# Kernel tuning notes

Measured on AMD Instinct MI355X. Metric: run time of the kernel, lower is better.

The kernel has to match this reference:

```python
import jax, jax.numpy as jnp
import numpy as np

ALPHA = 0.2          # LeakyReLU negative slope
NEG_BIG = -9e15      # mask value from the original code


def setup_inputs() -> dict:
    key = jax.random.key(0)
    k1, k2, k3, k4, k5 = jax.random.split(key, 5)
    N, Fin, Fout, C = 8192, 2048, 256, 8
    x = jax.random.normal(k1, (N, Fin), dtype=jnp.float32)
    # xavier_uniform-ish scale for params
    W = jax.random.normal(k2, (C, Fin, Fout), dtype=jnp.float32) / np.sqrt(Fin).astype(np.float32)
    a = jax.random.normal(k3, (2 * Fout, 1), dtype=jnp.float32) / np.sqrt(2 * Fout).astype(np.float32)
    cam_ids = jax.random.randint(k4, (N,), 0, C, dtype=jnp.int32)
    adj = jax.random.randint(k5, (N, N), 0, 2, dtype=jnp.int32)
    return {"x": x, "W": W, "a": a, "cam_ids": cam_ids, "adj": adj}


def reference(x, W, a, cam_ids, adj):
    N = x.shape[0]
    Fout = W.shape[-1]
    # per-node camera-specific projection: h[i] = x[i] @ W[cam_ids[i]]
    # compute all-camera projections (N, C, Fout) then gather per node;
    # avoids materializing W[cam_ids] of shape (N, Fin, Fout)
    hs = jnp.einsum('nd,cdo->nco', x, W)                       # (N, C, Fout)
    h = jnp.take_along_axis(hs, cam_ids[:, None, None], axis=1)[:, 0, :]  # (N, Fout)
    # e_ij = leakyrelu([h_i, h_j] @ a) = leakyrelu(h_i.a1 + h_j.a2)
    a1 = a[:Fout, 0]
    a2 = a[Fout:, 0]
    e = jax.nn.leaky_relu((h @ a1)[:, None] + (h @ a2)[None, :], ALPHA)  # (N, N)
    att = jnp.where(adj > 0, e, jnp.float32(NEG_BIG))
    att = jax.nn.softmax(att, axis=1)
    # dropout is identity at eval (p applied only in training)
    h_prime = att @ h                                          # (N, Fout)
    return jax.nn.elu(h_prime)                                 # concat=True -> ELU
```

## Files before the change

### kernel.cpp

```cpp
#include <hip/hip_runtime.h>

#define NR 8192
#define FIN 2048
#define FOUT 256
#define ALPHA 0.2f
#define NTMAX 136
#define KS 4
#define KLEN 512
#define NSTEPS 16
#define JC 4
#define NJ 2048

typedef float f32x4 __attribute__((ext_vector_type(4)));
typedef float f32x16 __attribute__((ext_vector_type(16)));
typedef int i32x4 __attribute__((ext_vector_type(4)));
typedef unsigned int u32x4 __attribute__((ext_vector_type(4)));
typedef unsigned short u16x4 __attribute__((ext_vector_type(4)));
typedef unsigned short u16x8 __attribute__((ext_vector_type(8)));
typedef __bf16 bf16x8 __attribute__((ext_vector_type(8)));
typedef _Float16 f16x8 __attribute__((ext_vector_type(8)));

__device__ __forceinline__ unsigned short f2bf(float f){
  unsigned u = __float_as_uint(f);
  return (unsigned short)((u + 0x7fffu + ((u >> 16) & 1u)) >> 16);
}
__device__ __forceinline__ float bf2f(unsigned short b){
  return __uint_as_float(((unsigned)b) << 16);
}
__device__ __forceinline__ void gload16(const void* gptr, void* lptr){
  __builtin_amdgcn_global_load_lds(
      (const __attribute__((address_space(1))) unsigned int*)gptr,
      (__attribute__((address_space(3))) unsigned int*)lptr, 16, 0, 0);
}

__global__ __launch_bounds__(256) void k_wth(const float* __restrict__ W,
                                             _Float16* __restrict__ WhT){
  __shared__ _Float16 tl[64][72];
  int t = threadIdx.x;
  int item = blockIdx.x;
  int k0 = (item & 31) << 6;
  int n0 = ((item >> 5) & 3) << 6;
  int c = item >> 7;
  {
    int kk = t >> 2, nq = (t & 3)*16;
    const float* src = W + ((size_t)c*FIN + k0 + kk)*FOUT + n0 + nq;
    #pragma unroll
    for (int q = 0; q < 4; q++){
      f32x4 v = *(const f32x4*)(src + q*4);
      #pragma unroll
      for (int e = 0; e < 4; e++) tl[nq + q*4 + e][kk] = (_Float16)v[e];
    }
  }
  __syncthreads();
  {
    int nn = t >> 2, kq = (t & 3)*16;
    union { u32x4 v[2]; _Float16 s[16]; } buf;
    #pragma unroll
    for (int e = 0; e < 16; e++) buf.s[e] = tl[nn][kq + e];
    u32x4* dst = (u32x4*)(WhT + ((size_t)c*FOUT + n0 + nn)*FIN + k0 + kq);
    dst[0] = buf.v[0]; dst[1] = buf.v[1];
  }
}

__global__ void k_bucket(const int* __restrict__ cam, int* __restrict__ prows,
                         int* __restrict__ tileCam){
  __shared__ int cnt[256][8];
  __shared__ int scnt[8];
  __shared__ int tst[9];
  int t = threadIdx.x;
  int loc[8];
  #pragma unroll
  for (int c = 0; c < 8; c++) loc[c] = 0;
  for (int k = 0; k < 32; k++) loc[cam[t*32 + k] & 7]++;
  #pragma unroll
  for (int c = 0; c < 8; c++) cnt[t][c] = loc[c];
  __syncthreads();
  if (t < 8){
    int s = 0;
    for (int i = 0; i < 256; i++){ int v = cnt[i][t]; cnt[i][t] = s; s += v; }
    scnt[t] = s;
  }
  __syncthreads();
  if (t == 0){
    int ts = 0;
    for (int c = 0; c < 8; c++){ tst[c] = ts; ts += (scnt[c] + 63) >> 6; }
    tst[8] = ts;
  }
  __syncthreads();
  for (int s = t; s < NTMAX*64; s += 256) prows[s] = -1;
  if (t < NTMAX){
    int tc = -1, te = tst[8];
    if (t < te){
      #pragma unroll
      for (int c = 0; c < 8; c++)
        if (t >= tst[c] && t < tst[c+1]) tc = c;
    }
    tileCam[t] = tc;
  }
  __syncthreads();
  int off[8];
  #pragma unroll
  for (int c = 0; c < 8; c++) off[c] = cnt[t][c];
  for (int k = 0; k < 32; k++){
    int n = t*32 + k; int c = cam[n] & 7;
    int slot = off[c]++;
    prows[(tst[c] + (slot >> 6))*64 + (slot & 63)] = n;
  }
}

__global__ __launch_bounds__(256, 3) void k_gmm(const float* __restrict__ x,
    const _Float16* __restrict__ WhT, const int* __restrict__ tileCam,
    const int* __restrict__ prows, float* __restrict__ partial){
  __shared__ __align__(16) char smem[41728];
  int item = blockIdx.x;
  int tile = item >> 2, ks = item & 3;
  int camc = tileCam[tile];
  if (camc < 0) return;
  _Float16* ab = (_Float16*)smem;
  int* rows  = (int*)(smem + 40960);
  int* growL = (int*)(smem + 41216);
  int t = threadIdx.x;
  if (t < 64){
    int r = prows[tile*64 + t];
    rows[t] = r; growL[t] = (r < 0) ? 0 : r;
  }
  __syncthreads();
  int lane = t & 63, w = t >> 6;
  int k0 = ks * KLEN;
  int wr = w >> 1, wc = w & 1;
  int rA = ((t >> 6) & 1)*32 + (t & 31);
  int koffA = (t >> 7)*16 + ((t >> 5) & 1)*8;
  const float* srcA = x + (size_t)growL[rA]*FIN + k0 + koffA;
  const _Float16* srcB[4];
  #pragma unroll
  for (int q = 0; q < 4; q++){
    int c2 = q*256 + t;
    int colg = ((c2 >> 6) & 7)*32 + (t & 31);
    srcB[q] = WhT + ((size_t)camc*FOUT + colg)*FIN + k0
            + (c2 >> 9)*16 + ((t >> 5) & 1)*8;
  }
  f32x16 acc[4];
  #pragma unroll
  for (int nb = 0; nb < 4; nb++)
    #pragma unroll
    for (int r = 0; r < 16; r++) acc[nb][r] = 0.f;
  int cur = 0;
  {
    f32x4 a0 = *(const f32x4*)srcA;
    f32x4 a1 = *(const f32x4*)(srcA + 4);
    #pragma unroll
    for (int q = 0; q < 4; q++) gload16(srcB[q], &ab[2048 + (q*256 + t)*8]);
    f16x8 hv;
    #pragma unroll
    for (int e = 0; e < 4; e++){ hv[e] = (_Float16)a0[e]; hv[4+e] = (_Float16)a1[e]; }
    *(f16x8*)&ab[t*8] = hv;
  }
  __syncthreads();
  for (int s = 0; s < NSTEPS; s++){
    bool have = (s + 1 < NSTEPS);
    int adv = have ? (s + 1)*32 : 0;
    f32x4 na0 = *(const f32x4*)(srcA + adv);
    f32x4 na1 = *(const f32x4*)(srcA + adv + 4);
    if (have){
      #pragma unroll
      for (int q = 0; q < 4; q++)
        gload16(srcB[q] + adv, &ab[(cur ^ 1)*10240 + 2048 + (q*256 + t)*8]);
    }
    const _Float16* base = ab + cur*10240;
    f16x8 af[2]; f16x8 bfr[2][4];
    #pragma unroll
    for (int kk = 0; kk < 2; kk++){
      af[kk] = *(const f16x8*)(base + ((kk*2 + wr)*64 + lane)*8);
      #pragma unroll
      for (int nb = 0; nb < 4; nb++)
        bfr[kk][nb] = *(const f16x8*)(base + 2048 + ((kk*8 + wc*4 + nb)*64 + lane)*8);
    }
    #pragma unroll
    for (int kk = 0; kk < 2; kk++)
      #pragma unroll
      for (int nb = 0; nb < 4; nb++)
        acc[nb] = __builtin_amdgcn_mfma_f32_32x32x16_f16(af[kk], bfr[kk][nb], acc[nb], 0, 0, 0);
    if (have){
      f16x8 hv;
      #pragma unroll
      for (int e = 0; e < 4; e++){ hv[e] = (_Float16)na0[e]; hv[4+e] = (_Float16)na1[e]; }
      *(f16x8*)&ab[(cur ^ 1)*10240 + t*8] = hv;
    }
    __syncthreads();
    cur ^= 1;
  }
  int colb = wc*128;
  #pragma unroll
  for (int nb = 0; nb < 4; nb++){
    #pragma unroll
    for (int r = 0; r < 16; r++){
      int rowl = wr*32 + (r & 3) + 8*(r >> 2) + 4*(lane >> 5);
      int grow = rows[rowl];
      if (grow >= 0)
        partial[((size_t)ks*NR + grow)*FOUT + colb + nb*32 + (lane & 31)] = acc[nb][r];
    }
  }
}

__global__ __launch_bounds__(256) void k_hsumT(const float* __restrict__ partial,
    const float* __restrict__ a, float* __restrict__ s1, float* __restrict__ s2,
    float* __restrict__ bm, unsigned short* __restrict__ hT){
  __shared__ __align__(16) char smem[36096];
  unsigned short* sums = (unsigned short*)smem;
  float* a1l = (float*)(smem + 33792);
  float* a2l = (float*)(smem + 34816);
  float* redv = (float*)(smem + 35840);
  int blk = blockIdx.x, t = threadIdx.x;
  int w = t >> 6, lane = t & 63;
  int r0 = blk*64;
  a1l[t] = a[t]; a2l[t] = a[FOUT + t];
  __syncthreads();
  float bmax = -3.0e38f;
  #pragma unroll
  for (int rep = 0; rep < 16; rep++){
    int row = rep*4 + w;
    const float* pp = partial + (size_t)(r0 + row)*FOUT + lane*4;
    f32x4 s; s[0] = s[1] = s[2] = s[3] = 0.f;
    #pragma unroll
    for (int ks = 0; ks < KS; ks++)
      s += *(const f32x4*)(pp + (size_t)ks*NR*FOUT);
    u16x4 pk;
    #pragma unroll
    for (int e = 0; e < 4; e++) pk[e] = f2bf(s[e]);
    *(u16x4*)&sums[row*264 + lane*4] = pk;
    f32x4 a1v = *(const f32x4*)&a1l[lane*4];
    f32x4 a2v = *(const f32x4*)&a2l[lane*4];
    float p1 = 0.f, p2 = 0.f;
    #pragma unroll
    for (int e = 0; e < 4; e++){ p1 = fmaf(s[e], a1v[e], p1); p2 = fmaf(s[e], a2v[e], p2); }
    #pragma unroll
    for (int off2 = 32; off2 > 0; off2 >>= 1){
      p1 += __shfl_xor(p1, off2);
      p2 += __shfl_xor(p2, off2);
    }
    if (lane == 0){
      s1[r0 + row] = p1; s2[r0 + row] = p2;
      bmax = fmaxf(bmax, p2);
    }
  }
  if (lane == 0) redv[w] = bmax;
  __syncthreads();
  if (t == 0)
    bm[blk] = fmaxf(fmaxf(redv[0], redv[1]), fmaxf(redv[2], redv[3]));
  int c = t;
  #pragma unroll
  for (int q = 0; q < 8; q++){
    u16x8 v;
    #pragma unroll
    for (int e = 0; e < 8; e++) v[e] = sums[(q*8 + e)*264 + c];
    *(u16x8*)(hT + (size_t)c*NR + r0 + q*8) = v;
  }
}

__global__ __launch_bounds__(512, 4) void k_flash(const int* __restrict__ adj,
    const float* __restrict__ s1g, const float* __restrict__ s2g,
    const float* __restrict__ bm, const unsigned short* __restrict__ hT,
    float* __restrict__ hp, float* __restrict__ Dp){
  __shared__ __align__(16) unsigned short hTl[256*64];
  __shared__ __align__(16) unsigned short pl[64][72];
  __shared__ float s1l[64], ml[64], Dl[64], red[8];
  int blk = blockIdx.x, t = threadIdx.x;
  int w = t >> 6, lane = t & 63;
  int it = blk & 127, jc = blk >> 7;
  int i0 = it*64;
  int jbase = jc * NJ;
  {
    float v = (t < 128) ? bm[t] : -3.0e38f;
    #pragma unroll
    for (int off = 32; off > 0; off >>= 1) v = fmaxf(v, __shfl_xor(v, off));
    if (lane == 0) red[w] = v;
  }
  __syncthreads();
  if (t == 0){
    float v = red[0];
    #pragma unroll
    for (int k = 1; k < 8; k++) v = fmaxf(v, red[k]);
    red[0] = v;
  }
  __syncthreads();
  float maxS2 = red[0];
  if (t < 64){
    float sv = s1g[i0 + t];
    s1l[t] = sv;
    float mm = sv + maxS2;
    ml[t] = fmaxf(mm, ALPHA*mm);
  }
  __syncthreads();
  int il = t >> 3, tj = t & 7;
  float s1i = s1l[il], mi = ml[il];
  float Dacc = 0.f;
  f32x16 acc0, acc1;
  #pragma unroll
  for (int k = 0; k < 16; k++){ acc0[k] = 0.f; acc1[k] = 0.f; }
  const unsigned short* hsrc[4];
  int ldst[4];
  #pragma unroll
  for (int q = 0; q < 4; q++){
    int g = t + 512*q;
    int row = g >> 3, part = g & 7;
    hsrc[q] = hT + (size_t)row*NR + jbase + part*8;
    ldst[q] = row*64 + ((part ^ (row & 7))*8);
  }
  const int* arow = adj + (size_t)(i0 + il)*NR + jbase + tj*8;
  u32x4 hch[4];
  #pragma unroll
  for (int q = 0; q < 4; q++) hch[q] = *(const u32x4*)hsrc[q];
  i32x4 ad0 = __builtin_nontemporal_load((const i32x4*)arow);
  i32x4 ad1 = __builtin_nontemporal_load(((const i32x4*)arow) + 1);
  f32x4 s20 = *(const f32x4*)(s2g + jbase + tj*8);
  f32x4 s21 = *(const f32x4*)(s2g + jbase + tj*8 + 4);
  for (int jt = 0; jt < NJ; jt += 64){
    u16x8 pu;
    float Dloc = 0.f;
    #pragma unroll
    for (int e = 0; e < 4; e++){
      float e0 = s1i + s20[e]; e0 = fmaxf(e0, ALPHA*e0);
      float p0 = (ad0[e] > 0) ? __expf(e0 - mi) : 0.f;
      unsigned short b0 = f2bf(p0); pu[e] = b0; Dloc += bf2f(b0);
      float e1 = s1i + s21[e]; e1 = fmaxf(e1, ALPHA*e1);
      float p1 = (ad1[e] > 0) ? __expf(e1 - mi) : 0.f;
      unsigned short b1 = f2bf(p1); pu[e + 4] = b1; Dloc += bf2f(b1);
    }
    Dacc += Dloc;
    *(u16x8*)&pl[il][tj*8] = pu;
    #pragma unroll
    for (int q = 0; q < 4; q++) *(u32x4*)&hTl[ldst[q]] = hch[q];
    __syncthreads();
    if (jt + 64 < NJ){
      #pragma unroll
      for (int q = 0; q < 4; q++){
        hsrc[q] += 64;
        hch[q] = *(const u32x4*)hsrc[q];
      }
      arow += 64;
      ad0 = __builtin_nontemporal_load((const i32x4*)arow);
      ad1 = __builtin_nontemporal_load(((const i32x4*)arow) + 1);
      s20 = *(const f32x4*)(s2g + jbase + jt + 64 + tj*8);
      s21 = *(const f32x4*)(s2g + jbase + jt + 64 + tj*8 + 4);
    }
    int nrow = w*32 + (lane & 31);
    #pragma unroll
    for (int ks = 0; ks < 4; ks++){
      int p = ks*2 + (lane >> 5);
      bf16x8 B = *(const bf16x8*)&hTl[nrow*64 + ((p ^ (nrow & 7))*8)];
      int koff = ks*16 + (lane >> 5)*8;
      bf16x8 a0 = *(const bf16x8*)&pl[lane & 31][koff];
      acc0 = __builtin_amdgcn_mfma_f32_32x32x16_bf16(a0, B, acc0, 0, 0, 0);
      bf16x8 a1 = *(const bf16x8*)&pl[32 + (lane & 31)][koff];
      acc1 = __builtin_amdgcn_mfma_f32_32x32x16_bf16(a1, B, acc1, 0, 0, 0);
    }
    __syncthreads();
  }
  Dacc += __shfl_xor(Dacc, 1);
  Dacc += __shfl_xor(Dacc, 2);
  Dacc += __shfl_xor(Dacc, 4);
  if (tj == 0) Dl[il] = Dacc;
  __syncthreads();
  if (t < 64) Dp[(size_t)jc*NR + i0 + t] = Dl[t];
  float* hpb = hp + (size_t)jc*NR*FOUT;
  int col = w*32 + (lane & 31);
  #pragma unroll
  for (int r = 0; r < 16; r++){
    int rowl = (r & 3) + 8*(r >> 2) + 4*(lane >> 5);
    hpb[(size_t)(i0 + rowl)*FOUT + col] = acc0[r];
    hpb[(size_t)(i0 + 32 + rowl)*FOUT + col] = acc1[r];
  }
}

__global__ __launch_bounds__(256) void k_final(const float* __restrict__ hp,
    const float* __restrict__ Dp, float* __restrict__ out){
  int g = blockIdx.x*256 + threadIdx.x;
  int i = g >> 6, cg4 = (g & 63)*4;
  f32x4 s; s[0] = s[1] = s[2] = s[3] = 0.f;
  float D = 0.f;
  #pragma unroll
  for (int jc = 0; jc < JC; jc++){
    s += *(const f32x4*)(hp + ((size_t)jc*NR + i)*FOUT + cg4);
    D += Dp[(size_t)jc*NR + i];
  }
  float inv = (D > 0.f) ? 1.f / D : 0.f;
  f32x4 o;
  #pragma unroll
  for (int e = 0; e < 4; e++){
    float v = s[e]*inv;
    o[e] = (v > 0.f) ? v : expm1f(v);
  }
  *(f32x4*)(out + (size_t)i*FOUT + cg4) = o;
}

extern "C" void kernel_launch(void* const* d_in, const int* in_sizes, int n_in,
                              void* d_out, int out_size, void* d_ws, size_t ws_size,
                              hipStream_t stream){
  (void)in_sizes; (void)n_in; (void)out_size; (void)ws_size;
  const float* x   = (const float*)d_in[0];
  const float* W   = (const float*)d_in[1];
  const float* a   = (const float*)d_in[2];
  const int*   cam = (const int*)d_in[3];
  const int*   adj = (const int*)d_in[4];
  float* out = (float*)d_out;
  char* ws = (char*)d_ws;

  size_t off = 0;
  auto alloc = [&](size_t b) -> void* {
    void* p = ws + off; off = (off + b + 255) & ~(size_t)255; return p;
  };
  int* tileCam  = (int*)alloc((size_t)NTMAX*4);
  int* prows    = (int*)alloc((size_t)NTMAX*64*4);
  _Float16* WhT = (_Float16*)alloc((size_t)8*FIN*FOUT*2);
  unsigned short* hT = (unsigned short*)alloc((size_t)NR*FOUT*2);
  float* s1 = (float*)alloc((size_t)NR*4);
  float* s2 = (float*)alloc((size_t)NR*4);
  float* bm = (float*)alloc(128*4);
  float* Dp = (float*)alloc((size_t)JC*NR*4);
  float* partial = (float*)alloc((size_t)KS*NR*FOUT*4);
  float* hp = partial;

  hipLaunchKernelGGL(k_wth, dim3(1024), dim3(256), 0, stream, W, WhT);
  hipLaunchKernelGGL(k_bucket, dim3(1), dim3(256), 0, stream,
                     cam, prows, tileCam);
  hipLaunchKernelGGL(k_gmm, dim3(NTMAX*4), dim3(256), 0, stream,
                     x, WhT, tileCam, prows, partial);
  hipLaunchKernelGGL(k_hsumT, dim3(128), dim3(256), 0, stream,
                     partial, a, s1, s2, bm, hT);
  hipLaunchKernelGGL(k_flash, dim3(512), dim3(512), 0, stream,
                     adj, s1, s2, bm, hT, hp, Dp);
  hipLaunchKernelGGL(k_final, dim3((NR*FOUT/4)/256), dim3(256), 0, stream,
                     hp, Dp, out);
}
```

Before: 199.4 us.

## Merge preprocessing kernels and fuse attention stages into a cooperative grid-synced kernel

Weight transpose and camera bucketing now run as one launch, with one extra block doing the bucketing. The hsum/transpose, flash-attention and final normalisation stages become phases of a single cooperative kernel separated by grid.sync(). The hsum phase moves to 512-thread blocks and the final phase processes two elements per thread. The aim is to cut kernel launch gaps and tail idling between the dependent stages. The cost is grid-wide barriers and the need for all 512 blocks to be resident at once; if the cooperative launch fails, it falls back to separate launches.

```diff
diff --git a/kernel.cpp b/kernel.cpp
--- a/kernel.cpp
+++ b/kernel.cpp
@@ -1,4 +1,7 @@
 #include <hip/hip_runtime.h>
+#include <hip/hip_cooperative_groups.h>
+
+namespace cg = cooperative_groups;
 
 #define NR 8192
 #define FIN 2048
@@ -33,11 +36,9 @@
       (__attribute__((address_space(3))) unsigned int*)lptr, 16, 0, 0);
 }
 
-__global__ __launch_bounds__(256) void k_wth(const float* __restrict__ W,
-                                             _Float16* __restrict__ WhT){
-  __shared__ _Float16 tl[64][72];
-  int t = threadIdx.x;
-  int item = blockIdx.x;
+__device__ __forceinline__ void phase_wth(int item, int t,
+    const float* __restrict__ W, _Float16* __restrict__ WhT, char* smem){
+  _Float16* tl = (_Float16*)smem;
   int k0 = (item & 31) << 6;
   int n0 = ((item >> 5) & 3) << 6;
   int c = item >> 7;
@@ -48,7 +49,7 @@
     for (int q = 0; q < 4; q++){
       f32x4 v = *(const f32x4*)(src + q*4);
       #pragma unroll
-      for (int e = 0; e < 4; e++) tl[nq + q*4 + e][kk] = (_Float16)v[e];
+      for (int e = 0; e < 4; e++) tl[(nq + q*4 + e)*72 + kk] = (_Float16)v[e];
     }
   }
   __syncthreads();
@@ -56,18 +57,17 @@
     int nn = t >> 2, kq = (t & 3)*16;
     union { u32x4 v[2]; _Float16 s[16]; } buf;
     #pragma unroll
-    for (int e = 0; e < 16; e++) buf.s[e] = tl[nn][kq + e];
+    for (int e = 0; e < 16; e++) buf.s[e] = tl[nn*72 + kq + e];
     u32x4* dst = (u32x4*)(WhT + ((size_t)c*FOUT + n0 + nn)*FIN + k0 + kq);
     dst[0] = buf.v[0]; dst[1] = buf.v[1];
   }
 }
 
-__global__ void k_bucket(const int* __restrict__ cam, int* __restrict__ prows,
-                         int* __restrict__ tileCam){
-  __shared__ int cnt[256][8];
-  __shared__ int scnt[8];
-  __shared__ int tst[9];
-  int t = threadIdx.x;
+__device__ __forceinline__ void phase_bucket(int t, const int* __restrict__ cam,
+    int* __restrict__ prows, int* __restrict__ tileCam, char* smem){
+  int (*cnt)[8] = (int(*)[8])smem;
+  int* scnt = (int*)(smem + 8192);
+  int* tst  = (int*)(smem + 8224);
   int loc[8];
   #pragma unroll
   for (int c = 0; c < 8; c++) loc[c] = 0;
@@ -106,6 +106,15 @@
     int slot = off[c]++;
     prows[(tst[c] + (slot >> 6))*64 + (slot & 63)] = n;
   }
+}
+
+__global__ __launch_bounds__(256) void k_pre(const float* __restrict__ W,
+    _Float16* __restrict__ WhT, const int* __restrict__ cam,
+    int* __restrict__ prows, int* __restrict__ tileCam){
+  __shared__ __align__(16) char smem[9216];
+  int blk = blockIdx.x, t = threadIdx.x;
+  if (blk < 1024) phase_wth(blk, t, W, WhT, smem);
+  else            phase_bucket(t, cam, prows, tileCam, smem);
 }
 
 __global__ __launch_bounds__(256, 3) void k_gmm(const float* __restrict__ x,
@@ -202,23 +211,22 @@
   }
 }
 
-__global__ __launch_bounds__(256) void k_hsumT(const float* __restrict__ partial,
-    const float* __restrict__ a, float* __restrict__ s1, float* __restrict__ s2,
-    float* __restrict__ bm, unsigned short* __restrict__ hT){
-  __shared__ __align__(16) char smem[36096];
+__device__ __forceinline__ void phase_hsumT512(int blk, int t,
+    const float* __restrict__ partial, const float* __restrict__ a,
+    float* __restrict__ s1, float* __restrict__ s2, float* __restrict__ bm,
+    unsigned short* __restrict__ hT, char* smem){
   unsigned short* sums = (unsigned short*)smem;
   float* a1l = (float*)(smem + 33792);
   float* a2l = (float*)(smem + 34816);
   float* redv = (float*)(smem + 35840);
-  int blk = blockIdx.x, t = threadIdx.x;
   int w = t >> 6, lane = t & 63;
   int r0 = blk*64;
-  a1l[t] = a[t]; a2l[t] = a[FOUT + t];
+  if (t < 256){ a1l[t] = a[t]; a2l[t] = a[FOUT + t]; }
   __syncthreads();
   float bmax = -3.0e38f;
   #pragma unroll
-  for (int rep = 0; rep < 16; rep++){
-    int row = rep*4 + w;
+  for (int rep = 0; rep < 8; rep++){
+    int row = rep*8 + w;
     const float* pp = partial + (size_t)(r0 + row)*FOUT + lane*4;
     f32x4 s; s[0] = s[1] = s[2] = s[3] = 0.f;
     #pragma unroll
@@ -245,26 +253,33 @@
   }
   if (lane == 0) redv[w] = bmax;
   __syncthreads();
-  if (t == 0)
-    bm[blk] = fmaxf(fmaxf(redv[0], redv[1]), fmaxf(redv[2], redv[3]));
-  int c = t;
-  #pragma unroll
-  for (int q = 0; q < 8; q++){
+  if (t == 0){
+    float v = redv[0];
+    #pragma unroll
+    for (int k = 1; k < 8; k++) v = fmaxf(v, redv[k]);
+    bm[blk] = v;
+  }
+  int c = t & 255, qb = (t >> 8)*4;
+  #pragma unroll
+  for (int q = 0; q < 4; q++){
     u16x8 v;
     #pragma unroll
-    for (int e = 0; e < 8; e++) v[e] = sums[(q*8 + e)*264 + c];
-    *(u16x8*)(hT + (size_t)c*NR + r0 + q*8) = v;
-  }
-}
-
-__global__ __launch_bounds__(512, 4) void k_flash(const int* __restrict__ adj,
-    const float* __restrict__ s1g, const float* __restrict__ s2g,
-    const float* __restrict__ bm, const unsigned short* __restrict__ hT,
-    float* __restrict__ hp, float* __restrict__ Dp){
-  __shared__ __align__(16) unsigned short hTl[256*64];
-  __shared__ __align__(16) unsigned short pl[64][72];
-  __shared__ float s1l[64], ml[64], Dl[64], red[8];
-  int blk = blockIdx.x, t = threadIdx.x;
+    for (int e = 0; e < 8; e++) v[e] = sums[((qb + q)*8 + e)*264 + c];
+    *(u16x8*)(hT + (size_t)c*NR + r0 + (qb + q)*8) = v;
+  }
+}
+
+__device__ __forceinline__ void phase_flash(int blk, int t,
+    const int* __restrict__ adj, const float* __restrict__ s1g,
+    const float* __restrict__ s2g, const float* __restrict__ bm,
+    const unsigned short* __restrict__ hT, float* __restrict__ hp,
+    float* __restrict__ Dp, char* smem){
+  unsigned short* hTl = (unsigned short*)smem;
+  unsigned short (*pl)[72] = (unsigned short(*)[72])(smem + 32768);
+  float* s1l = (float*)(smem + 41984);
+  float* ml  = (float*)(smem + 42240);
+  float* Dl  = (float*)(smem + 42496);
+  float* red = (float*)(smem + 42752);
   int w = t >> 6, lane = t & 63;
   int it = blk & 127, jc = blk >> 7;
   int i0 = it*64;
@@ -372,25 +387,59 @@
   }
 }
 
-__global__ __launch_bounds__(256) void k_final(const float* __restrict__ hp,
-    const float* __restrict__ Dp, float* __restrict__ out){
-  int g = blockIdx.x*256 + threadIdx.x;
-  int i = g >> 6, cg4 = (g & 63)*4;
-  f32x4 s; s[0] = s[1] = s[2] = s[3] = 0.f;
-  float D = 0.f;
-  #pragma unroll
-  for (int jc = 0; jc < JC; jc++){
-    s += *(const f32x4*)(hp + ((size_t)jc*NR + i)*FOUT + cg4);
-    D += Dp[(size_t)jc*NR + i];
-  }
-  float inv = (D > 0.f) ? 1.f / D : 0.f;
-  f32x4 o;
-  #pragma unroll
-  for (int e = 0; e < 4; e++){
-    float v = s[e]*inv;
-    o[e] = (v > 0.f) ? v : expm1f(v);
-  }
-  *(f32x4*)(out + (size_t)i*FOUT + cg4) = o;
+__device__ __forceinline__ void phase_final2(int gid,
+    const float* __restrict__ hp, const float* __restrict__ Dp,
+    float* __restrict__ out){
+  #pragma unroll
+  for (int rep = 0; rep < 2; rep++){
+    int u = rep*262144 + gid;
+    int i = u >> 6, cg4 = (u & 63)*4;
+    f32x4 s; s[0] = s[1] = s[2] = s[3] = 0.f;
+    float D = 0.f;
+    #pragma unroll
+    for (int jc = 0; jc < JC; jc++){
+      s += *(const f32x4*)(hp + ((size_t)jc*NR + i)*FOUT + cg4);
+      D += Dp[(size_t)jc*NR + i];
+    }
+    float inv = (D > 0.f) ? 1.f / D : 0.f;
+    f32x4 o;
+    #pragma unroll
+    for (int e = 0; e < 4; e++){
+      float v = s[e]*inv;
+      o[e] = (v > 0.f) ? v : expm1f(v);
+    }
+    *(f32x4*)(out + (size_t)i*FOUT + cg4) = o;
+  }
+}
+
+__global__ __launch_bounds__(512, 4) void kCoop(const float* partial,
+    const float* a, float* s1, float* s2, float* bm, unsigned short* hT,
+    const int* adj, float* hp, float* Dp, float* out){
+  __shared__ __align__(16) char smem[43008];
+  cg::grid_group grid = cg::this_grid();
+  int blk = blockIdx.x, t = threadIdx.x;
+  if (blk < 128) phase_hsumT512(blk, t, partial, a, s1, s2, bm, hT, smem);
+  __syncthreads();
+  grid.sync();
+  phase_flash(blk, t, adj, s1, s2, bm, hT, hp, Dp, smem);
+  grid.sync();
+  phase_final2(blk*512 + t, hp, Dp, out);
+}
+
+__global__ __launch_bounds__(512) void kF_hsumT(const float* partial,
+    const float* a, float* s1, float* s2, float* bm, unsigned short* hT){
+  __shared__ __align__(16) char smem[36096];
+  phase_hsumT512(blockIdx.x, threadIdx.x, partial, a, s1, s2, bm, hT, smem);
+}
+__global__ __launch_bounds__(512, 4) void kF_flash(const int* adj,
+    const float* s1, const float* s2, const float* bm,
+    const unsigned short* hT, float* hp, float* Dp){
+  __shared__ __align__(16) char smem[43008];
+  phase_flash(blockIdx.x, threadIdx.x, adj, s1, s2, bm, hT, hp, Dp, smem);
+}
+__global__ __launch_bounds__(512) void kF_final(const float* hp,
+    const float* Dp, float* out){
+  phase_final2(blockIdx.x*512 + threadIdx.x, hp, Dp, out);
 }
 
 extern "C" void kernel_launch(void* const* d_in, const int* in_sizes, int n_in,
@@ -420,15 +469,23 @@
   float* partial = (float*)alloc((size_t)KS*NR*FOUT*4);
   float* hp = partial;
 
-  hipLaunchKernelGGL(k_wth, dim3(1024), dim3(256), 0, stream, W, WhT);
-  hipLaunchKernelGGL(k_bucket, dim3(1), dim3(256), 0, stream,
-                     cam, prows, tileCam);
+  hipLaunchKernelGGL(k_pre, dim3(1025), dim3(256), 0, stream,
+                     W, WhT, cam, prows, tileCam);
   hipLaunchKernelGGL(k_gmm, dim3(NTMAX*4), dim3(256), 0, stream,
                      x, WhT, tileCam, prows, partial);
-  hipLaunchKernelGGL(k_hsumT, dim3(128), dim3(256), 0, stream,
-                     partial, a, s1, s2, bm, hT);
-  hipLaunchKernelGGL(k_flash, dim3(512), dim3(512), 0, stream,
-                     adj, s1, s2, bm, hT, hp, Dp);
-  hipLaunchKernelGGL(k_final, dim3((NR*FOUT/4)/256), dim3(256), 0, stream,
-                     hp, Dp, out);
-}
+  {
+    void* args[] = { (void*)&partial, (void*)&a, (void*)&s1, (void*)&s2,
+                     (void*)&bm, (void*)&hT, (void*)&adj, (void*)&hp,
+                     (void*)&Dp, (void*)&out };
+    hipError_t rc = hipLaunchCooperativeKernel((const void*)kCoop, dim3(512),
+                                               dim3(512), args, 0, stream);
+    if (rc != hipSuccess){
+      hipLaunchKernelGGL(kF_hsumT, dim3(128), dim3(512), 0, stream,
+                         partial, a, s1, s2, bm, hT);
+      hipLaunchKernelGGL(kF_flash, dim3(512), dim3(512), 0, stream,
+                         adj, s1, s2, bm, hT, hp, Dp);
+      hipLaunchKernelGGL(kF_final, dim3(512), dim3(512), 0, stream,
+                         hp, Dp, out);
+    }
+  }
+}
```

Measured after the change: 319.6 us. +60.3%, slower.

## Split flash attention over eight key chunks with swizzled P tile and fewer barriers

Applied to the files above, without the earlier changes.

Doubles the number of key-column chunks in the attention kernel (1024 blocks of 512 threads, each covering 1024 columns) and raises the occupancy hint. It also swizzles the P tile in LDS instead of padding it, computes the global max and per-row values directly from global memory without the startup barriers, and writes the row sums without an LDS round trip. The aim is to fill more CUs and cut sync and bank-conflict overhead. In exchange the partial-output buffer doubles in size, the final reduction reads twice as much, and register pressure is tighter at the higher occupancy target.

```diff
diff --git a/kernel.cpp b/kernel.cpp
--- a/kernel.cpp
+++ b/kernel.cpp
@@ -8,8 +8,8 @@
 #define KS 4
 #define KLEN 512
 #define NSTEPS 16
-#define JC 4
-#define NJ 2048
+#define JC 8
+#define NJ 1024
 
 typedef float f32x4 __attribute__((ext_vector_type(4)));
 typedef float f32x16 __attribute__((ext_vector_type(16)));
@@ -257,42 +257,27 @@
   }
 }
 
-__global__ __launch_bounds__(512, 4) void k_flash(const int* __restrict__ adj,
+__global__ __launch_bounds__(512, 8) void k_flash(const int* __restrict__ adj,
     const float* __restrict__ s1g, const float* __restrict__ s2g,
     const float* __restrict__ bm, const unsigned short* __restrict__ hT,
     float* __restrict__ hp, float* __restrict__ Dp){
   __shared__ __align__(16) unsigned short hTl[256*64];
-  __shared__ __align__(16) unsigned short pl[64][72];
-  __shared__ float s1l[64], ml[64], Dl[64], red[8];
+  __shared__ __align__(16) unsigned short pl[64*64];
   int blk = blockIdx.x, t = threadIdx.x;
   int w = t >> 6, lane = t & 63;
   int it = blk & 127, jc = blk >> 7;
   int i0 = it*64;
   int jbase = jc * NJ;
-  {
-    float v = (t < 128) ? bm[t] : -3.0e38f;
-    #pragma unroll
-    for (int off = 32; off > 0; off >>= 1) v = fmaxf(v, __shfl_xor(v, off));
-    if (lane == 0) red[w] = v;
-  }
-  __syncthreads();
-  if (t == 0){
-    float v = red[0];
-    #pragma unroll
-    for (int k = 1; k < 8; k++) v = fmaxf(v, red[k]);
-    red[0] = v;
-  }
-  __syncthreads();
-  float maxS2 = red[0];
-  if (t < 64){
-    float sv = s1g[i0 + t];
-    s1l[t] = sv;
-    float mm = sv + maxS2;
-    ml[t] = fmaxf(mm, ALPHA*mm);
-  }
-  __syncthreads();
+  float maxS2 = -3.0e38f;
+  #pragma unroll
+  for (int q = 0; q < 32; q++){
+    f32x4 v = *(const f32x4*)(bm + q*4);
+    maxS2 = fmaxf(fmaxf(maxS2, fmaxf(v[0], v[1])), fmaxf(v[2], v[3]));
+  }
   int il = t >> 3, tj = t & 7;
-  float s1i = s1l[il], mi = ml[il];
+  float s1i = s1g[i0 + il];
+  float mm = s1i + maxS2;
+  float mi = fmaxf(mm, ALPHA*mm);
   float Dacc = 0.f;
   f32x16 acc0, acc1;
   #pragma unroll
@@ -306,6 +291,7 @@
     hsrc[q] = hT + (size_t)row*NR + jbase + part*8;
     ldst[q] = row*64 + ((part ^ (row & 7))*8);
   }
+  int plw = il*64 + ((tj ^ (il & 7))*8);
   const int* arow = adj + (size_t)(i0 + il)*NR + jbase + tj*8;
   u32x4 hch[4];
   #pragma unroll
@@ -327,16 +313,13 @@
       unsigned short b1 = f2bf(p1); pu[e + 4] = b1; Dloc += bf2f(b1);
     }
     Dacc += Dloc;
-    *(u16x8*)&pl[il][tj*8] = pu;
+    *(u16x8*)&pl[plw] = pu;
     #pragma unroll
     for (int q = 0; q < 4; q++) *(u32x4*)&hTl[ldst[q]] = hch[q];
     __syncthreads();
     if (jt + 64 < NJ){
       #pragma unroll
-      for (int q = 0; q < 4; q++){
-        hsrc[q] += 64;
-        hch[q] = *(const u32x4*)hsrc[q];
-      }
+      for (int q = 0; q < 4; q++) hch[q] = *(const u32x4*)(hsrc[q] + jt + 64);
       arow += 64;
       ad0 = __builtin_nontemporal_load((const i32x4*)arow);
       ad1 = __builtin_nontemporal_load(((const i32x4*)arow) + 1);
@@ -344,14 +327,14 @@
       s21 = *(const f32x4*)(s2g + jbase + jt + 64 + tj*8 + 4);
     }
     int nrow = w*32 + (lane & 31);
+    int r = lane & 31;
     #pragma unroll
     for (int ks = 0; ks < 4; ks++){
       int p = ks*2 + (lane >> 5);
       bf16x8 B = *(const bf16x8*)&hTl[nrow*64 + ((p ^ (nrow & 7))*8)];
-      int koff = ks*16 + (lane >> 5)*8;
-      bf16x8 a0 = *(const bf16x8*)&pl[lane & 31][koff];
+      bf16x8 a0 = *(const bf16x8*)&pl[r*64 + ((p ^ (r & 7))*8)];
       acc0 = __builtin_amdgcn_mfma_f32_32x32x16_bf16(a0, B, acc0, 0, 0, 0);
-      bf16x8 a1 = *(const bf16x8*)&pl[32 + (lane & 31)][koff];
+      bf16x8 a1 = *(const bf16x8*)&pl[(32 + r)*64 + ((p ^ (r & 7))*8)];
       acc1 = __builtin_amdgcn_mfma_f32_32x32x16_bf16(a1, B, acc1, 0, 0, 0);
     }
     __syncthreads();
@@ -359,16 +342,14 @@
   Dacc += __shfl_xor(Dacc, 1);
   Dacc += __shfl_xor(Dacc, 2);
   Dacc += __shfl_xor(Dacc, 4);
-  if (tj == 0) Dl[il] = Dacc;
-  __syncthreads();
-  if (t < 64) Dp[(size_t)jc*NR + i0 + t] = Dl[t];
+  if (tj == 0) Dp[(size_t)jc*NR + i0 + il] = Dacc;
   float* hpb = hp + (size_t)jc*NR*FOUT;
   int col = w*32 + (lane & 31);
   #pragma unroll
-  for (int r = 0; r < 16; r++){
-    int rowl = (r & 3) + 8*(r >> 2) + 4*(lane >> 5);
-    hpb[(size_t)(i0 + rowl)*FOUT + col] = acc0[r];
-    hpb[(size_t)(i0 + 32 + rowl)*FOUT + col] = acc1[r];
+  for (int r2 = 0; r2 < 16; r2++){
+    int rowl = (r2 & 3) + 8*(r2 >> 2) + 4*(lane >> 5);
+    hpb[(size_t)(i0 + rowl)*FOUT + col] = acc0[r2];
+    hpb[(size_t)(i0 + 32 + rowl)*FOUT + col] = acc1[r2];
   }
 }
 
@@ -417,8 +398,11 @@
   float* s2 = (float*)alloc((size_t)NR*4);
   float* bm = (float*)alloc(128*4);
   float* Dp = (float*)alloc((size_t)JC*NR*4);
-  float* partial = (float*)alloc((size_t)KS*NR*FOUT*4);
-  float* hp = partial;
+  size_t sh1 = (size_t)KS*NR*FOUT*4;
+  size_t sh2 = (size_t)JC*NR*FOUT*4;
+  void* shared = alloc(sh1 > sh2 ? sh1 : sh2);
+  float* partial = (float*)shared;
+  float* hp      = (float*)shared;
 
   hipLaunchKernelGGL(k_wth, dim3(1024), dim3(256), 0, stream, W, WhT);
   hipLaunchKernelGGL(k_bucket, dim3(1), dim3(256), 0, stream,
@@ -427,7 +411,7 @@
                      x, WhT, tileCam, prows, partial);
   hipLaunchKernelGGL(k_hsumT, dim3(128), dim3(256), 0, stream,
                      partial, a, s1, s2, bm, hT);
-  hipLaunchKernelGGL(k_flash, dim3(512), dim3(512), 0, stream,
+  hipLaunchKernelGGL(k_flash, dim3(1024), dim3(512), 0, stream,
                      adj, s1, s2, bm, hT, hp, Dp);
   hipLaunchKernelGGL(k_final, dim3((NR*FOUT/4)/256), dim3(256), 0, stream,
                      hp, Dp, out);
```

Result: slower. 685.0 us (+243.5%).

## Halve flash attention row tile to 32 rows with 256-thread blocks

Applied to the files above, without the earlier changes.

The flash kernel now processes 32 query rows per block with 4 waves instead of 64 rows with 8 waves, doubling the grid to 1024 blocks. Each wave now computes two 32-column output slabs sharing one A fragment, and each thread loads 8 hT chunks per step instead of 4. This raises the block count for better CU occupancy and load balance, but each block re-streams the full hT tile for only half the rows, doubling hT traffic per output row.

```diff
diff --git a/kernel.cpp b/kernel.cpp
--- a/kernel.cpp
+++ b/kernel.cpp
@@ -257,17 +257,17 @@
   }
 }
 
-__global__ __launch_bounds__(512, 4) void k_flash(const int* __restrict__ adj,
+__global__ __launch_bounds__(256, 4) void k_flash(const int* __restrict__ adj,
     const float* __restrict__ s1g, const float* __restrict__ s2g,
     const float* __restrict__ bm, const unsigned short* __restrict__ hT,
     float* __restrict__ hp, float* __restrict__ Dp){
   __shared__ __align__(16) unsigned short hTl[256*64];
-  __shared__ __align__(16) unsigned short pl[64][72];
-  __shared__ float s1l[64], ml[64], Dl[64], red[8];
+  __shared__ __align__(16) unsigned short pl[32][72];
+  __shared__ float s1l[32], ml[32], red[4];
   int blk = blockIdx.x, t = threadIdx.x;
   int w = t >> 6, lane = t & 63;
-  int it = blk & 127, jc = blk >> 7;
-  int i0 = it*64;
+  int it = blk & 255, jc = blk >> 8;
+  int i0 = it*32;
   int jbase = jc * NJ;
   {
     float v = (t < 128) ? bm[t] : -3.0e38f;
@@ -276,15 +276,11 @@
     if (lane == 0) red[w] = v;
   }
   __syncthreads();
-  if (t == 0){
-    float v = red[0];
-    #pragma unroll
-    for (int k = 1; k < 8; k++) v = fmaxf(v, red[k]);
-    red[0] = v;
-  }
+  if (t == 0)
+    red[0] = fmaxf(fmaxf(red[0], red[1]), fmaxf(red[2], red[3]));
   __syncthreads();
   float maxS2 = red[0];
-  if (t < 64){
+  if (t < 32){
     float sv = s1g[i0 + t];
     s1l[t] = sv;
     float mm = sv + maxS2;
@@ -297,19 +293,14 @@
   f32x16 acc0, acc1;
   #pragma unroll
   for (int k = 0; k < 16; k++){ acc0[k] = 0.f; acc1[k] = 0.f; }
-  const unsigned short* hsrc[4];
-  int ldst[4];
-  #pragma unroll
-  for (int q = 0; q < 4; q++){
-    int g = t + 512*q;
-    int row = g >> 3, part = g & 7;
-    hsrc[q] = hT + (size_t)row*NR + jbase + part*8;
-    ldst[q] = row*64 + ((part ^ (row & 7))*8);
-  }
+  int r0s = t >> 3, part = t & 7;
+  const unsigned short* hbase = hT + (size_t)r0s*NR + jbase + part*8;
+  int ldst0 = r0s*64 + ((part ^ (r0s & 7))*8);
   const int* arow = adj + (size_t)(i0 + il)*NR + jbase + tj*8;
-  u32x4 hch[4];
-  #pragma unroll
-  for (int q = 0; q < 4; q++) hch[q] = *(const u32x4*)hsrc[q];
+  u32x4 hch[8];
+  #pragma unroll
+  for (int q = 0; q < 8; q++)
+    hch[q] = *(const u32x4*)(hbase + (size_t)q*(32*NR));
   i32x4 ad0 = __builtin_nontemporal_load((const i32x4*)arow);
   i32x4 ad1 = __builtin_nontemporal_load(((const i32x4*)arow) + 1);
   f32x4 s20 = *(const f32x4*)(s2g + jbase + tj*8);
@@ -329,46 +320,48 @@
     Dacc += Dloc;
     *(u16x8*)&pl[il][tj*8] = pu;
     #pragma unroll
-    for (int q = 0; q < 4; q++) *(u32x4*)&hTl[ldst[q]] = hch[q];
+    for (int q = 0; q < 8; q++) *(u32x4*)&hTl[ldst0 + q*2048] = hch[q];
     __syncthreads();
     if (jt + 64 < NJ){
-      #pragma unroll
-      for (int q = 0; q < 4; q++){
-        hsrc[q] += 64;
-        hch[q] = *(const u32x4*)hsrc[q];
-      }
+      int jn = jt + 64;
+      #pragma unroll
+      for (int q = 0; q < 8; q++)
+        hch[q] = *(const u32x4*)(hbase + jn + (size_t)q*(32*NR));
       arow += 64;
       ad0 = __builtin_nontemporal_load((const i32x4*)arow);
       ad1 = __builtin_nontemporal_load(((const i32x4*)arow) + 1);
-      s20 = *(const f32x4*)(s2g + jbase + jt + 64 + tj*8);
-      s21 = *(const f32x4*)(s2g + jbase + jt + 64 + tj*8 + 4);
-    }
-    int nrow = w*32 + (lane & 31);
+      s20 = *(const f32x4*)(s2g + jbase + jn + tj*8);
+      s21 = *(const f32x4*)(s2g + jbase + jn + tj*8 + 4);
+    }
+    int r = lane & 31, hi = lane >> 5;
+    int nrow0 = w*64 + r;
+    int nrow1 = w*64 + 32 + r;
     #pragma unroll
     for (int ks = 0; ks < 4; ks++){
-      int p = ks*2 + (lane >> 5);
-      bf16x8 B = *(const bf16x8*)&hTl[nrow*64 + ((p ^ (nrow & 7))*8)];
-      int koff = ks*16 + (lane >> 5)*8;
-      bf16x8 a0 = *(const bf16x8*)&pl[lane & 31][koff];
-      acc0 = __builtin_amdgcn_mfma_f32_32x32x16_bf16(a0, B, acc0, 0, 0, 0);
-      bf16x8 a1 = *(const bf16x8*)&pl[32 + (lane & 31)][koff];
-      acc1 = __builtin_amdgcn_mfma_f32_32x32x16_bf16(a1, B, acc1, 0, 0, 0);
+      int p = ks*2 + hi;
+      int koff = ks*16 + hi*8;
+      bf16x8 a = *(const bf16x8*)&pl[r][koff];
+      bf16x8 B0 = *(const bf16x8*)&hTl[nrow0*64 + ((p ^ (nrow0 & 7))*8)];
+      acc0 = __builtin_amdgcn_mfma_f32_32x32x16_bf16(a, B0, acc0, 0, 0, 0);
+      bf16x8 B1 = *(const bf16x8*)&hTl[nrow1*64 + ((p ^ (nrow1 & 7))*8)];
+      acc1 = __builtin_amdgcn_mfma_f32_32x32x16_bf16(a, B1, acc1, 0, 0, 0);
     }
     __syncthreads();
   }
   Dacc += __shfl_xor(Dacc, 1);
   Dacc += __shfl_xor(Dacc, 2);
   Dacc += __shfl_xor(Dacc, 4);
-  if (tj == 0) Dl[il] = Dacc;
-  __syncthreads();
-  if (t < 64) Dp[(size_t)jc*NR + i0 + t] = Dl[t];
+  if (tj == 0) Dp[(size_t)jc*NR + i0 + il] = Dacc;
   float* hpb = hp + (size_t)jc*NR*FOUT;
-  int col = w*32 + (lane & 31);
-  #pragma unroll
-  for (int r = 0; r < 16; r++){
-    int rowl = (r & 3) + 8*(r >> 2) + 4*(lane >> 5);
-    hpb[(size_t)(i0 + rowl)*FOUT + col] = acc0[r];
-    hpb[(size_t)(i0 + 32 + rowl)*FOUT + col] = acc1[r];
+  {
+    int r = lane & 31, hi = lane >> 5;
+    int col0 = w*64 + r, col1 = w*64 + 32 + r;
+    #pragma unroll
+    for (int e = 0; e < 16; e++){
+      int rowl = (e & 3) + 8*(e >> 2) + 4*hi;
+      hpb[(size_t)(i0 + rowl)*FOUT + col0] = acc0[e];
+      hpb[(size_t)(i0 + rowl)*FOUT + col1] = acc1[e];
+    }
   }
 }
 
@@ -427,7 +420,7 @@
                      x, WhT, tileCam, prows, partial);
   hipLaunchKernelGGL(k_hsumT, dim3(128), dim3(256), 0, stream,
                      partial, a, s1, s2, bm, hT);
-  hipLaunchKernelGGL(k_flash, dim3(512), dim3(512), 0, stream,
+  hipLaunchKernelGGL(k_flash, dim3(1024), dim3(256), 0, stream,
                      adj, s1, s2, bm, hT, hp, Dp);
   hipLaunchKernelGGL(k_final, dim3((NR*FOUT/4)/256), dim3(256), 0, stream,
                      hp, Dp, out);
```

Result: no change. 200.5 us (+0.5%).
